# Performance work log

Hardware: AMD Instinct MI355X
Metric: run time of the kernel (lower is better)

The kernel has to match this reference:

```python
import jax, jax.numpy as jnp
import numpy as np

Z, P, CIN, COUT, E, HID = 4, 512, 32, 32, 65536, 128

def setup_inputs() -> dict:
    key = jax.random.key(0)
    ks = jax.random.split(key, 8)
    return {
        "features": jax.random.normal(ks[0], (Z, P, CIN), dtype=jnp.float32),
        "edge_vec": jax.random.normal(ks[1], (E, 3), dtype=jnp.float32),
        "W1": jax.random.normal(ks[2], (4, HID), dtype=jnp.float32) * 0.5,
        "b1": jax.random.normal(ks[3], (HID,), dtype=jnp.float32) * 0.1,
        "W2": jax.random.normal(ks[4], (HID, COUT * CIN), dtype=jnp.float32) * (1.0 / np.sqrt(HID)),
        "edge_batch": jax.random.randint(ks[5], (E,), 0, Z),
        "edge_a": jax.random.randint(ks[6], (E,), 0, P),
        "edge_b": jax.random.randint(ks[7], (E,), 0, P),
        "n_norm": 1,
    }

def reference(features, edge_vec, W1, b1, W2, edge_batch, edge_a, edge_b, n_norm):
    Zb, Pn, Cin = features.shape
    # zero near-degenerate radii (matches radius[norm < 1e-10] = 0)
    r = jnp.linalg.norm(edge_vec, axis=-1, keepdims=True)  # [E,1]
    vec = jnp.where(r < 1e-10, jnp.zeros_like(edge_vec), edge_vec)
    rn = jnp.where(r < 1e-10, jnp.zeros_like(r), r)
    # per-edge kernel: MLP(vec, |vec|) -> [E, c_out, c_in]
    x = jnp.concatenate([vec, rn], axis=-1)               # [E,4]
    h = jax.nn.relu(x @ W1 + b1)                          # [E,HID]
    Cout = W2.shape[1] // Cin
    k = (h @ W2).reshape(-1, Cout, Cin)                   # [E,co,ci]
    # gather neighbor features, per-edge matvec, scatter-add to centers
    f_b = features[edge_batch, edge_b]                    # [E,ci]
    msg = jnp.einsum('eij,ej->ei', k, f_b)                # [E,co]
    seg = edge_batch * Pn + edge_a
    out = jax.ops.segment_sum(msg, seg, num_segments=Zb * Pn)
    out = out.reshape(Zb, Pn, Cout)
    return out / jnp.sqrt(jnp.asarray(n_norm, dtype=features.dtype))
```

## Files before the change

kernel.cpp:

```cpp
#include <hip/hip_runtime.h>
#include <hip/hip_bf16.h>

#define ZBATCH 4
#define PN     512
#define CINC   32
#define COUTC  32
#define EN     65536
#define HIDN   128
#define NNODE  (ZBATCH*PN)
#define JD     (HIDN*COUTC)
#define CAP    128

__global__ void bin_k(const int* __restrict__ eb, const int* __restrict__ ea,
                      const int* __restrict__ ebn,
                      int* __restrict__ cnt_src, int* __restrict__ cnt_dst,
                      int* __restrict__ order_src, int* __restrict__ order_dst) {
  const int e = blockIdx.x * 256 + threadIdx.x;
  const int zb = eb[e];
  const int ns = zb * PN + ebn[e];
  const int nd = zb * PN + ea[e];
  const int p = atomicAdd(&cnt_src[ns], 1);
  if (p < CAP) order_src[ns * CAP + p] = e;
  const int q = atomicAdd(&cnt_dst[nd], 1);
  if (q < CAP) order_dst[nd * CAP + q] = e;
}

__global__ __launch_bounds__(256) void pass1_k(const float* __restrict__ F,
                                               const float* __restrict__ W2,
                                               __hip_bfloat16* __restrict__ Wf) {
  const int t = threadIdx.x;
  const int j = blockIdx.x * 256 + t;
  const int n0 = blockIdx.y * 16;
  const int h = j >> 5, co = j & 31;
  const float4* w4 = (const float4*)(W2 + h * (COUTC * CINC) + co * CINC);
  float w[32];
#pragma unroll
  for (int q = 0; q < 8; ++q) {
    const float4 x = w4[q];
    w[4 * q] = x.x; w[4 * q + 1] = x.y; w[4 * q + 2] = x.z; w[4 * q + 3] = x.w;
  }
  for (int n = 0; n < 16; ++n) {
    const float* fr = F + (size_t)(n0 + n) * CINC;
    float acc = 0.f;
#pragma unroll
    for (int ci = 0; ci < 32; ++ci) acc = fmaf(fr[ci], w[ci], acc);
    Wf[(size_t)(n0 + n) * JD + j] = __float2bfloat16(acc);
  }
}

__global__ __launch_bounds__(256) void pass2m_k(
    const float* __restrict__ evec, const float* __restrict__ W1,
    const float* __restrict__ b1, const __hip_bfloat16* __restrict__ Wf,
    const int* __restrict__ cnt_src, const int* __restrict__ order_src,
    const int* __restrict__ nn, float* __restrict__ msg) {
  const int n = blockIdx.x;
  const int t = threadIdx.x;
  const int lane = t & 63;
  const int w = t >> 6;
  const int co = lane & 31;
  const int hh = lane >> 5;

  __shared__ float w1s[4][HIDN];
  __shared__ float b1s[HIDN];
  __shared__ __align__(16) float Hbuf[4][8][HIDN];

  const int count0 = cnt_src[n];
  const int count = count0 < CAP ? count0 : CAP;
  if (count == 0) return;

  for (int i = t; i < 4 * HIDN; i += 256) w1s[i >> 7][i & 127] = W1[i];
  for (int i = t; i < HIDN; i += 256) b1s[i] = b1[i];

  float wf[64];
  {
    const __hip_bfloat16* wp = Wf + (size_t)n * JD + hh * 64 * COUTC + co;
#pragma unroll
    for (int j = 0; j < 64; ++j) wf[j] = __bfloat162float(wp[(size_t)j * COUTC]);
  }
  const float scale = rsqrtf((float)nn[0]);
  __syncthreads();

  const int h0 = lane << 1;
  const int* ord = order_src + (size_t)n * CAP;
  for (int base = w * 8; base < count; base += 32) {
    const int nb = (count - base < 8) ? (count - base) : 8;
    for (int i = 0; i < nb; ++i) {
      const int e = ord[base + i];
      const float x0 = evec[3 * e], x1 = evec[3 * e + 1], x2 = evec[3 * e + 2];
      const float r = sqrtf(x0 * x0 + x1 * x1 + x2 * x2);
      const bool bad = (r < 1e-10f);
      const float y0 = bad ? 0.f : x0, y1 = bad ? 0.f : x1;
      const float y2 = bad ? 0.f : x2, y3 = bad ? 0.f : r;
      float a0 = b1s[h0]     + y0 * w1s[0][h0]     + y1 * w1s[1][h0]
                             + y2 * w1s[2][h0]     + y3 * w1s[3][h0];
      float a1 = b1s[h0 + 1] + y0 * w1s[0][h0 + 1] + y1 * w1s[1][h0 + 1]
                             + y2 * w1s[2][h0 + 1] + y3 * w1s[3][h0 + 1];
      float2 hv;
      hv.x = fmaxf(a0, 0.f);
      hv.y = fmaxf(a1, 0.f);
      *(float2*)(&Hbuf[w][i][h0]) = hv;
    }
    __builtin_amdgcn_wave_barrier();
    for (int i = 0; i < nb; ++i) {
      const int e = ord[base + i];
      const float* hp = &Hbuf[w][i][hh * 64];
      float acc = 0.f;
#pragma unroll
      for (int k = 0; k < 16; ++k) {
        const float4 h4 = *(const float4*)(hp + 4 * k);
        acc = fmaf(h4.x, wf[4 * k],     acc);
        acc = fmaf(h4.y, wf[4 * k + 1], acc);
        acc = fmaf(h4.z, wf[4 * k + 2], acc);
        acc = fmaf(h4.w, wf[4 * k + 3], acc);
      }
      acc += __shfl_xor(acc, 32);
      if (hh == 0) msg[(size_t)e * COUTC + co] = acc * scale;
    }
    __builtin_amdgcn_wave_barrier();
  }
}

__global__ __launch_bounds__(64) void reduce_k(const float* __restrict__ msg,
                                               const int* __restrict__ cnt_dst,
                                               const int* __restrict__ order_dst,
                                               float* __restrict__ out) {
  const int n = blockIdx.x;
  const int t = threadIdx.x;
  const int co = t & 31;
  const int hh = t >> 5;
  __shared__ int idxs[CAP];
  const int c0 = cnt_dst[n];
  const int count = c0 < CAP ? c0 : CAP;
  for (int i = t; i < count; i += 64) idxs[i] = order_dst[(size_t)n * CAP + i];
  __syncthreads();
  float acc = 0.f;
#pragma unroll 4
  for (int i = hh; i < count; i += 2) acc += msg[(size_t)idxs[i] * COUTC + co];
  acc += __shfl_xor(acc, 32);
  if (t < 32) out[(size_t)n * COUTC + co] = acc;
}

extern "C" void kernel_launch(void* const* d_in, const int* in_sizes, int n_in,
                              void* d_out, int out_size, void* d_ws, size_t ws_size,
                              hipStream_t stream) {
  const float* features   = (const float*)d_in[0];
  const float* edge_vec   = (const float*)d_in[1];
  const float* W1         = (const float*)d_in[2];
  const float* b1         = (const float*)d_in[3];
  const float* W2         = (const float*)d_in[4];
  const int*   edge_batch = (const int*)d_in[5];
  const int*   edge_a     = (const int*)d_in[6];
  const int*   edge_b     = (const int*)d_in[7];
  const int*   n_norm     = (const int*)d_in[8];
  float* out = (float*)d_out;

  char* ws = (char*)d_ws;
  __hip_bfloat16* Wf = (__hip_bfloat16*)ws;
  float* msg = (float*)(ws + (size_t)NNODE * JD * 2);
  int* ints = (int*)(ws + (size_t)NNODE * JD * 2 + (size_t)EN * COUTC * 4);
  int* cnt_src   = ints;
  int* cnt_dst   = ints + NNODE;
  int* order_src = ints + 2 * NNODE;
  int* order_dst = ints + 2 * NNODE + NNODE * CAP;
  const size_t need = (size_t)NNODE * JD * 2 + (size_t)EN * COUTC * 4
                    + (size_t)(2 * NNODE + 2 * NNODE * CAP) * 4;
  if (ws_size < need) return;

  hipMemsetAsync(cnt_src, 0, 2 * NNODE * 4, stream);
  bin_k<<<EN / 256, 256, 0, stream>>>(edge_batch, edge_a, edge_b,
                                      cnt_src, cnt_dst, order_src, order_dst);
  pass1_k<<<dim3(16, 128), 256, 0, stream>>>(features, W2, Wf);
  pass2m_k<<<NNODE, 256, 0, stream>>>(edge_vec, W1, b1, Wf, cnt_src, order_src,
                                      n_norm, msg);
  reduce_k<<<NNODE, 64, 0, stream>>>(msg, cnt_dst, order_dst, out);
}
```

Measured before the change: 148.3 us.

## Fuse binning with Wf precompute, batch edge loads, widen reduce blocks

Merges the edge-binning kernel and the feature-weight precompute into one launch using block-index ranges, removing one kernel launch. The message kernel caches edge indices in shared memory, loads eight edge vectors up front with clamped indices, and splits the dot product into four independent accumulators to expose more memory and FMA parallelism. The reduction kernel packs four nodes per 256-thread block, one per wave, and uses four partial sums per lane. Padding the last batch with duplicated edges does redundant work but only writes valid ones.

Result: faster. 144.6 us (-2.5%).

```diff
diff --git a/kernel.cpp b/kernel.cpp
--- a/kernel.cpp
+++ b/kernel.cpp
@@ -11,26 +11,28 @@
 #define JD     (HIDN*COUTC)
 #define CAP    128
 
-__global__ void bin_k(const int* __restrict__ eb, const int* __restrict__ ea,
-                      const int* __restrict__ ebn,
-                      int* __restrict__ cnt_src, int* __restrict__ cnt_dst,
-                      int* __restrict__ order_src, int* __restrict__ order_dst) {
-  const int e = blockIdx.x * 256 + threadIdx.x;
-  const int zb = eb[e];
-  const int ns = zb * PN + ebn[e];
-  const int nd = zb * PN + ea[e];
-  const int p = atomicAdd(&cnt_src[ns], 1);
-  if (p < CAP) order_src[ns * CAP + p] = e;
-  const int q = atomicAdd(&cnt_dst[nd], 1);
-  if (q < CAP) order_dst[nd * CAP + q] = e;
-}
-
-__global__ __launch_bounds__(256) void pass1_k(const float* __restrict__ F,
-                                               const float* __restrict__ W2,
-                                               __hip_bfloat16* __restrict__ Wf) {
+__global__ __launch_bounds__(256) void k1_bin_wf(
+    const float* __restrict__ F, const float* __restrict__ W2,
+    __hip_bfloat16* __restrict__ Wf, const int* __restrict__ eb,
+    const int* __restrict__ ea, const int* __restrict__ ebn,
+    int* __restrict__ cnt_src, int* __restrict__ cnt_dst,
+    int* __restrict__ order_src, int* __restrict__ order_dst) {
   const int t = threadIdx.x;
-  const int j = blockIdx.x * 256 + t;
-  const int n0 = blockIdx.y * 16;
+  const int b = blockIdx.x;
+  if (b < 256) {
+    const int e = b * 256 + t;
+    const int zb = eb[e];
+    const int ns = zb * PN + ebn[e];
+    const int nd = zb * PN + ea[e];
+    const int p = atomicAdd(&cnt_src[ns], 1);
+    if (p < CAP) order_src[ns * CAP + p] = e;
+    const int q = atomicAdd(&cnt_dst[nd], 1);
+    if (q < CAP) order_dst[nd * CAP + q] = e;
+    return;
+  }
+  const int bb = b - 256;
+  const int j = (bb & 15) * 256 + t;
+  const int n0 = (bb >> 4) * 16;
   const int h = j >> 5, co = j & 31;
   const float4* w4 = (const float4*)(W2 + h * (COUTC * CINC) + co * CINC);
   float w[32];
@@ -48,28 +50,28 @@
   }
 }
 
-__global__ __launch_bounds__(256) void pass2m_k(
+__global__ __launch_bounds__(256) void k2_msg(
     const float* __restrict__ evec, const float* __restrict__ W1,
     const float* __restrict__ b1, const __hip_bfloat16* __restrict__ Wf,
     const int* __restrict__ cnt_src, const int* __restrict__ order_src,
     const int* __restrict__ nn, float* __restrict__ msg) {
   const int n = blockIdx.x;
   const int t = threadIdx.x;
-  const int lane = t & 63;
-  const int w = t >> 6;
-  const int co = lane & 31;
-  const int hh = lane >> 5;
+  const int lane = t & 63, w = t >> 6;
+  const int co = lane & 31, hh = lane >> 5;
 
   __shared__ float w1s[4][HIDN];
   __shared__ float b1s[HIDN];
+  __shared__ int ords[CAP];
   __shared__ __align__(16) float Hbuf[4][8][HIDN];
 
-  const int count0 = cnt_src[n];
-  const int count = count0 < CAP ? count0 : CAP;
+  const int c0 = cnt_src[n];
+  const int count = c0 < CAP ? c0 : CAP;
   if (count == 0) return;
 
   for (int i = t; i < 4 * HIDN; i += 256) w1s[i >> 7][i & 127] = W1[i];
   for (int i = t; i < HIDN; i += 256) b1s[i] = b1[i];
+  if (t < count) ords[t] = order_src[(size_t)n * CAP + t];
 
   float wf[64];
   {
@@ -81,16 +83,25 @@
   __syncthreads();
 
   const int h0 = lane << 1;
-  const int* ord = order_src + (size_t)n * CAP;
   for (int base = w * 8; base < count; base += 32) {
-    const int nb = (count - base < 8) ? (count - base) : 8;
-    for (int i = 0; i < nb; ++i) {
-      const int e = ord[base + i];
-      const float x0 = evec[3 * e], x1 = evec[3 * e + 1], x2 = evec[3 * e + 2];
-      const float r = sqrtf(x0 * x0 + x1 * x1 + x2 * x2);
+    int e8[8]; float ex[8], ey[8], ez[8];
+#pragma unroll
+    for (int i = 0; i < 8; ++i) {
+      const int idx = (base + i < count) ? (base + i) : (count - 1);
+      e8[i] = ords[idx];
+    }
+#pragma unroll
+    for (int i = 0; i < 8; ++i) {
+      ex[i] = evec[3 * e8[i]];
+      ey[i] = evec[3 * e8[i] + 1];
+      ez[i] = evec[3 * e8[i] + 2];
+    }
+#pragma unroll
+    for (int i = 0; i < 8; ++i) {
+      const float r = sqrtf(ex[i] * ex[i] + ey[i] * ey[i] + ez[i] * ez[i]);
       const bool bad = (r < 1e-10f);
-      const float y0 = bad ? 0.f : x0, y1 = bad ? 0.f : x1;
-      const float y2 = bad ? 0.f : x2, y3 = bad ? 0.f : r;
+      const float y0 = bad ? 0.f : ex[i], y1 = bad ? 0.f : ey[i];
+      const float y2 = bad ? 0.f : ez[i], y3 = bad ? 0.f : r;
       float a0 = b1s[h0]     + y0 * w1s[0][h0]     + y1 * w1s[1][h0]
                              + y2 * w1s[2][h0]     + y3 * w1s[3][h0];
       float a1 = b1s[h0 + 1] + y0 * w1s[0][h0 + 1] + y1 * w1s[1][h0 + 1]
@@ -101,43 +112,58 @@
       *(float2*)(&Hbuf[w][i][h0]) = hv;
     }
     __builtin_amdgcn_wave_barrier();
-    for (int i = 0; i < nb; ++i) {
-      const int e = ord[base + i];
-      const float* hp = &Hbuf[w][i][hh * 64];
-      float acc = 0.f;
-#pragma unroll
-      for (int k = 0; k < 16; ++k) {
-        const float4 h4 = *(const float4*)(hp + 4 * k);
-        acc = fmaf(h4.x, wf[4 * k],     acc);
-        acc = fmaf(h4.y, wf[4 * k + 1], acc);
-        acc = fmaf(h4.z, wf[4 * k + 2], acc);
-        acc = fmaf(h4.w, wf[4 * k + 3], acc);
+#pragma unroll
+    for (int i = 0; i < 8; ++i) {
+      const float4* hp = (const float4*)(&Hbuf[w][i][hh * 64]);
+      float a0 = 0.f, a1 = 0.f, a2 = 0.f, a3 = 0.f;
+#pragma unroll
+      for (int k = 0; k < 4; ++k) {
+        const float4 p0 = hp[4 * k + 0];
+        const float4 p1 = hp[4 * k + 1];
+        const float4 p2 = hp[4 * k + 2];
+        const float4 p3 = hp[4 * k + 3];
+        a0 = fmaf(p0.x, wf[16 * k + 0], a0);  a0 = fmaf(p0.y, wf[16 * k + 1], a0);
+        a0 = fmaf(p0.z, wf[16 * k + 2], a0);  a0 = fmaf(p0.w, wf[16 * k + 3], a0);
+        a1 = fmaf(p1.x, wf[16 * k + 4], a1);  a1 = fmaf(p1.y, wf[16 * k + 5], a1);
+        a1 = fmaf(p1.z, wf[16 * k + 6], a1);  a1 = fmaf(p1.w, wf[16 * k + 7], a1);
+        a2 = fmaf(p2.x, wf[16 * k + 8], a2);  a2 = fmaf(p2.y, wf[16 * k + 9], a2);
+        a2 = fmaf(p2.z, wf[16 * k + 10], a2); a2 = fmaf(p2.w, wf[16 * k + 11], a2);
+        a3 = fmaf(p3.x, wf[16 * k + 12], a3); a3 = fmaf(p3.y, wf[16 * k + 13], a3);
+        a3 = fmaf(p3.z, wf[16 * k + 14], a3); a3 = fmaf(p3.w, wf[16 * k + 15], a3);
       }
+      float acc = (a0 + a1) + (a2 + a3);
       acc += __shfl_xor(acc, 32);
-      if (hh == 0) msg[(size_t)e * COUTC + co] = acc * scale;
+      if (hh == 0 && base + i < count)
+        msg[(size_t)e8[i] * COUTC + co] = acc * scale;
     }
     __builtin_amdgcn_wave_barrier();
   }
 }
 
-__global__ __launch_bounds__(64) void reduce_k(const float* __restrict__ msg,
-                                               const int* __restrict__ cnt_dst,
-                                               const int* __restrict__ order_dst,
-                                               float* __restrict__ out) {
-  const int n = blockIdx.x;
+__global__ __launch_bounds__(256) void k3_reduce(
+    const float* __restrict__ msg, const int* __restrict__ cnt_dst,
+    const int* __restrict__ order_dst, float* __restrict__ out) {
   const int t = threadIdx.x;
-  const int co = t & 31;
-  const int hh = t >> 5;
-  __shared__ int idxs[CAP];
+  const int lane = t & 63, w = t >> 6;
+  const int co = lane & 31, hh = lane >> 5;
+  const int n = blockIdx.x * 4 + w;
+  __shared__ int idxs[4][CAP];
   const int c0 = cnt_dst[n];
   const int count = c0 < CAP ? c0 : CAP;
-  for (int i = t; i < count; i += 64) idxs[i] = order_dst[(size_t)n * CAP + i];
-  __syncthreads();
-  float acc = 0.f;
-#pragma unroll 4
-  for (int i = hh; i < count; i += 2) acc += msg[(size_t)idxs[i] * COUTC + co];
+  for (int i = lane; i < count; i += 64)
+    idxs[w][i] = order_dst[(size_t)n * CAP + i];
+  __builtin_amdgcn_wave_barrier();
+  float a0 = 0.f, a1 = 0.f, a2 = 0.f, a3 = 0.f;
+  for (int g = hh * 4; g < count; g += 8) {
+    const int i1 = g + 1, i2 = g + 2, i3 = g + 3;
+    a0 += msg[(size_t)idxs[w][g] * COUTC + co];
+    if (i1 < count) a1 += msg[(size_t)idxs[w][i1] * COUTC + co];
+    if (i2 < count) a2 += msg[(size_t)idxs[w][i2] * COUTC + co];
+    if (i3 < count) a3 += msg[(size_t)idxs[w][i3] * COUTC + co];
+  }
+  float acc = (a0 + a1) + (a2 + a3);
   acc += __shfl_xor(acc, 32);
-  if (t < 32) out[(size_t)n * COUTC + co] = acc;
+  if (hh == 0) out[(size_t)n * COUTC + co] = acc;
 }
 
 extern "C" void kernel_launch(void* const* d_in, const int* in_sizes, int n_in,
@@ -161,16 +187,16 @@
   int* cnt_src   = ints;
   int* cnt_dst   = ints + NNODE;
   int* order_src = ints + 2 * NNODE;
-  int* order_dst = ints + 2 * NNODE + NNODE * CAP;
+  int* order_dst = order_src + NNODE * CAP;
   const size_t need = (size_t)NNODE * JD * 2 + (size_t)EN * COUTC * 4
                     + (size_t)(2 * NNODE + 2 * NNODE * CAP) * 4;
   if (ws_size < need) return;
 
   hipMemsetAsync(cnt_src, 0, 2 * NNODE * 4, stream);
-  bin_k<<<EN / 256, 256, 0, stream>>>(edge_batch, edge_a, edge_b,
-                                      cnt_src, cnt_dst, order_src, order_dst);
-  pass1_k<<<dim3(16, 128), 256, 0, stream>>>(features, W2, Wf);
-  pass2m_k<<<NNODE, 256, 0, stream>>>(edge_vec, W1, b1, Wf, cnt_src, order_src,
-                                      n_norm, msg);
-  reduce_k<<<NNODE, 64, 0, stream>>>(msg, cnt_dst, order_dst, out);
-}
+  k1_bin_wf<<<256 + 2048, 256, 0, stream>>>(features, W2, Wf, edge_batch,
+                                            edge_a, edge_b, cnt_src, cnt_dst,
+                                            order_src, order_dst);
+  k2_msg<<<NNODE, 256, 0, stream>>>(edge_vec, W1, b1, Wf, cnt_src, order_src,
+                                    n_norm, msg);
+  k3_reduce<<<NNODE / 4, 256, 0, stream>>>(msg, cnt_dst, order_dst, out);
+}
```
